# Performance work log

Measured on AMD Instinct MI355X. Metric: run time of the kernel, lower is better.

Reference implementation:

```python
import jax, jax.numpy as jnp
import numpy as np

NEG_INF = -1e9

def setup_inputs() -> dict:
    key = jax.random.key(0)
    ks = jax.random.split(key, 6)
    B, M, RNN, H, D = 64, 1024, 1024, 512, 2048
    return {
        "h": jax.random.normal(ks[0], (B, RNN), dtype=jnp.float32),
        "att_feats": jax.random.normal(ks[1], (B, M, D), dtype=jnp.float32),
        "att_mask": jax.random.randint(ks[2], (B, M), 0, 2, dtype=jnp.int32),
        "p_att_feats": jax.random.normal(ks[3], (B, M, H), dtype=jnp.float32),
        "W_ah": jax.random.normal(ks[4], (H, RNN), dtype=jnp.float32) * (1.0 / np.sqrt(RNN)),
        "w_alpha": jax.random.normal(ks[5], (H,), dtype=jnp.float32) * (1.0 / np.sqrt(H)),
    }

def reference(h, att_feats, att_mask, p_att_feats, W_ah, w_alpha):
    # Wah(h): [B, H]
    wah = h @ W_ah.T
    # additive attention energies: tanh(Wah(h)[:, None, :] + p_att_feats) -> [B, M, H]
    e = jnp.tanh(wah[:, None, :] + p_att_feats)
    # project to scalar per region: [B, M]
    logits = jnp.einsum("bmh,h->bm", e, w_alpha)
    logits = jnp.where(att_mask == 0, NEG_INF, logits)
    alpha = jax.nn.softmax(logits, axis=-1)
    # weighted sum of region features: [B, D]
    att = jnp.einsum("bm,bmd->bd", alpha, att_feats)
    return att
```

## Files before the change

### kernel.cpp

```cpp
#include <hip/hip_runtime.h>
#include <math.h>

#define B   64
#define M   1024
#define RNN 1024
#define H   512
#define D   2048

#define NCHUNK 16
#define CROWS  (M / NCHUNK)
#define RPW    (CROWS / 4)

__device__ __forceinline__ float fast_tanh(float x) {
    float ax = fabsf(x);
    float t  = __expf(-2.0f * ax);
    float r  = (1.0f - t) * __builtin_amdgcn_rcpf(1.0f + t);
    return copysignf(r, x);
}

__global__ __launch_bounds__(256) void k_wah(const float* __restrict__ h,
                                             const float* __restrict__ W,
                                             float* __restrict__ wah) {
    const int tid = threadIdx.x, lane = tid & 63, w = tid >> 6;
    const int bt = blockIdx.y * 16;
    const int j0 = blockIdx.x * 8 + w * 2;

    __shared__ float s_h[16 * RNN];
    const float4* h4  = (const float4*)(h + (size_t)bt * RNN);
    float4*       sh4 = (float4*)s_h;
#pragma unroll
    for (int k = 0; k < 16; ++k)
        sh4[tid + k * 256] = h4[tid + k * 256];

    const float4* Wa = (const float4*)(W + (size_t)j0 * RNN);
    const float4* Wb = (const float4*)(W + (size_t)(j0 + 1) * RNN);
    float4 wa[4], wb[4];
#pragma unroll
    for (int k = 0; k < 4; ++k) { wa[k] = Wa[lane + 64 * k]; wb[k] = Wb[lane + 64 * k]; }
    __syncthreads();

    for (int b = 0; b < 16; ++b) {
        float d0 = 0.0f, d1 = 0.0f;
#pragma unroll
        for (int k = 0; k < 4; ++k) {
            float4 hv = sh4[b * 256 + lane + 64 * k];
            d0 += hv.x * wa[k].x + hv.y * wa[k].y + hv.z * wa[k].z + hv.w * wa[k].w;
            d1 += hv.x * wb[k].x + hv.y * wb[k].y + hv.z * wb[k].z + hv.w * wb[k].w;
        }
#pragma unroll
        for (int off = 32; off > 0; off >>= 1) {
            d0 += __shfl_xor(d0, off);
            d1 += __shfl_xor(d1, off);
        }
        if (lane == 0)
            *(float2*)(wah + (size_t)(bt + b) * H + j0) = make_float2(d0, d1);
    }
}

__global__ __launch_bounds__(256) void k_fused(const float* __restrict__ wah,
                                               const float* __restrict__ p_att,
                                               const int* __restrict__ mask,
                                               const float* __restrict__ w_alpha,
                                               const float* __restrict__ feats,
                                               float* __restrict__ partial,
                                               float* __restrict__ zpart) {
    const int b   = blockIdx.x;
    const int c   = blockIdx.y;
    const int tid = threadIdx.x;
    const int lane = tid & 63;
    const int w    = tid >> 6;

    __shared__ float          s_w[CROWS];
    __shared__ float          s_zred[4];
    __shared__ unsigned short s_idx[CROWS + 4];
    __shared__ float          s_val[CROWS + 4];
    __shared__ int            s_cntreal;

    const float4* wh4 = (const float4*)(wah + (size_t)b * H);
    const float4* wa4 = (const float4*)w_alpha;
    float4 wh0 = wh4[lane], wh1 = wh4[lane + 64];
    float4 wa0 = wa4[lane], wa1 = wa4[lane + 64];

    const int     m0   = c * CROWS;
    const int*    mrow = mask + (size_t)b * M + m0;
    const float4* pb4  = (const float4*)(p_att + ((size_t)b * M + m0) * H);

    float zsum = 0.0f;
    for (int r = w * RPW; r < w * RPW + RPW; ++r) {
        float e = 0.0f;
        if (mrow[r] != 0) {
            float4 p0 = pb4[(size_t)r * (H / 4) + lane];
            float4 p1 = pb4[(size_t)r * (H / 4) + 64 + lane];
            float s = fast_tanh(p0.x + wh0.x) * wa0.x
                    + fast_tanh(p0.y + wh0.y) * wa0.y
                    + fast_tanh(p0.z + wh0.z) * wa0.z
                    + fast_tanh(p0.w + wh0.w) * wa0.w
                    + fast_tanh(p1.x + wh1.x) * wa1.x
                    + fast_tanh(p1.y + wh1.y) * wa1.y
                    + fast_tanh(p1.z + wh1.z) * wa1.z
                    + fast_tanh(p1.w + wh1.w) * wa1.w;
#pragma unroll
            for (int off = 32; off > 0; off >>= 1)
                s += __shfl_xor(s, off);
            e = __expf(s);
        }
        if (lane == 0) s_w[r] = e;
        zsum += e;
    }
    if (lane == 0) s_zred[w] = zsum;
    __syncthreads();
    if (tid == 0)
        zpart[(size_t)c * B + b] = (s_zred[0] + s_zred[1]) + (s_zred[2] + s_zred[3]);

    if (tid < CROWS) {
        float a = s_w[tid];
        bool pred = (a != 0.0f);
        unsigned long long bal = __ballot(pred);
        int pos = __popcll(bal & ((1ull << lane) - 1ull));
        if (pred) { s_idx[pos] = (unsigned short)tid; s_val[pos] = a; }
        if (lane == 0) s_cntreal = __popcll(bal);
    }
    __syncthreads();
    const int cnt = s_cntreal;
    const int n   = (cnt + 3) & ~3;
    if (tid >= cnt && tid < n) {
        s_idx[tid] = (cnt > 0) ? s_idx[cnt - 1] : (unsigned short)0;
        s_val[tid] = 0.0f;
    }
    __syncthreads();

    const float4* fb4 = (const float4*)(feats + ((size_t)b * M + m0) * D)
                        + (size_t)w * 128 + lane;
    float4 acc0 = {0.f, 0.f, 0.f, 0.f}, acc1 = {0.f, 0.f, 0.f, 0.f};
    for (int i = 0; i < n; i += 4) {
        int   r0 = s_idx[i],     r1 = s_idx[i + 1];
        int   r2 = s_idx[i + 2], r3 = s_idx[i + 3];
        float v0 = s_val[i],     v1 = s_val[i + 1];
        float v2 = s_val[i + 2], v3 = s_val[i + 3];
        const float4* q0 = fb4 + (size_t)r0 * (D / 4);
        const float4* q1 = fb4 + (size_t)r1 * (D / 4);
        const float4* q2 = fb4 + (size_t)r2 * (D / 4);
        const float4* q3 = fb4 + (size_t)r3 * (D / 4);
        float4 f00 = q0[0], f01 = q0[64];
        float4 f10 = q1[0], f11 = q1[64];
        float4 f20 = q2[0], f21 = q2[64];
        float4 f30 = q3[0], f31 = q3[64];
        acc0.x += v0 * f00.x; acc0.y += v0 * f00.y; acc0.z += v0 * f00.z; acc0.w += v0 * f00.w;
        acc1.x += v0 * f01.x; acc1.y += v0 * f01.y; acc1.z += v0 * f01.z; acc1.w += v0 * f01.w;
        acc0.x += v1 * f10.x; acc0.y += v1 * f10.y; acc0.z += v1 * f10.z; acc0.w += v1 * f10.w;
        acc1.x += v1 * f11.x; acc1.y += v1 * f11.y; acc1.z += v1 * f11.z; acc1.w += v1 * f11.w;
        acc0.x += v2 * f20.x; acc0.y += v2 * f20.y; acc0.z += v2 * f20.z; acc0.w += v2 * f20.w;
        acc1.x += v2 * f21.x; acc1.y += v2 * f21.y; acc1.z += v2 * f21.z; acc1.w += v2 * f21.w;
        acc0.x += v3 * f30.x; acc0.y += v3 * f30.y; acc0.z += v3 * f30.z; acc0.w += v3 * f30.w;
        acc1.x += v3 * f31.x; acc1.y += v3 * f31.y; acc1.z += v3 * f31.z; acc1.w += v3 * f31.w;
    }
    float4* ob = (float4*)(partial + ((size_t)c * B + b) * D) + (size_t)w * 128 + lane;
    ob[0]  = acc0;
    ob[64] = acc1;
}

__global__ __launch_bounds__(256) void k_reduce(const float* __restrict__ partial,
                                                const float* __restrict__ zpart,
                                                float* __restrict__ out) {
    int i4 = blockIdx.x * 256 + threadIdx.x;
    int b  = i4 >> 9;
    float Z = 0.0f;
#pragma unroll
    for (int c = 0; c < NCHUNK; ++c)
        Z += zpart[c * B + b];
    const float4* p4 = (const float4*)partial;
    float4 s = p4[i4];
#pragma unroll
    for (int c = 1; c < NCHUNK; ++c) {
        float4 v = p4[(size_t)c * (B * D / 4) + i4];
        s.x += v.x; s.y += v.y; s.z += v.z; s.w += v.w;
    }
    float inv = 1.0f / Z;
    float4 r = {s.x * inv, s.y * inv, s.z * inv, s.w * inv};
    ((float4*)out)[i4] = r;
}

extern "C" void kernel_launch(void* const* d_in, const int* in_sizes, int n_in,
                              void* d_out, int out_size, void* d_ws, size_t ws_size,
                              hipStream_t stream) {
    const float* h       = (const float*)d_in[0];
    const float* feats   = (const float*)d_in[1];
    const int*   mask    = (const int*)d_in[2];
    const float* p_att   = (const float*)d_in[3];
    const float* W_ah    = (const float*)d_in[4];
    const float* w_alpha = (const float*)d_in[5];
    float* out = (float*)d_out;

    float* ws      = (float*)d_ws;
    float* wah     = ws;
    float* zpart   = wah + B * H;
    float* partial = zpart + NCHUNK * B;

    k_wah   <<<dim3(H / 8, B / 16), 256, 0, stream>>>(h, W_ah, wah);
    k_fused <<<dim3(B, NCHUNK), 256, 0, stream>>>(wah, p_att, mask, w_alpha, feats,
                                                  partial, zpart);
    k_reduce<<<dim3(B * D / 1024), 256, 0, stream>>>(partial, zpart, out);
}
```

Before: 78.63 us.

## Fuse feature gather into the score loop with per-wave full-row accumulation

The fused kernel now issues the att_feats row loads alongside the p_att loads and accumulates e*feats inside the same per-row loop. Each wave owns whole rows and keeps 32 accumulator floats per lane across all of D, and the four waves are combined through a 32KB shared-memory reduction. This removes the two-phase scheme with its score buffer, ballot compaction and extra barriers, and overlaps feature loads with the tanh work. In exchange, register pressure and shared memory rise (launch bounds now ask for 4 blocks), and each wave walks its rows serially.

```diff
diff --git a/kernel.cpp b/kernel.cpp
--- a/kernel.cpp
+++ b/kernel.cpp
@@ -57,24 +57,21 @@
     }
 }
 
-__global__ __launch_bounds__(256) void k_fused(const float* __restrict__ wah,
-                                               const float* __restrict__ p_att,
-                                               const int* __restrict__ mask,
-                                               const float* __restrict__ w_alpha,
-                                               const float* __restrict__ feats,
-                                               float* __restrict__ partial,
-                                               float* __restrict__ zpart) {
+__global__ __launch_bounds__(256, 4) void k_fused(const float* __restrict__ wah,
+                                                  const float* __restrict__ p_att,
+                                                  const int* __restrict__ mask,
+                                                  const float* __restrict__ w_alpha,
+                                                  const float* __restrict__ feats,
+                                                  float* __restrict__ partial,
+                                                  float* __restrict__ zpart) {
     const int b   = blockIdx.x;
     const int c   = blockIdx.y;
     const int tid = threadIdx.x;
     const int lane = tid & 63;
     const int w    = tid >> 6;
 
-    __shared__ float          s_w[CROWS];
-    __shared__ float          s_zred[4];
-    __shared__ unsigned short s_idx[CROWS + 4];
-    __shared__ float          s_val[CROWS + 4];
-    __shared__ int            s_cntreal;
+    __shared__ float s_acc[4][D];
+    __shared__ float s_z[4];
 
     const float4* wh4 = (const float4*)(wah + (size_t)b * H);
     const float4* wa4 = (const float4*)w_alpha;
@@ -84,79 +81,60 @@
     const int     m0   = c * CROWS;
     const int*    mrow = mask + (size_t)b * M + m0;
     const float4* pb4  = (const float4*)(p_att + ((size_t)b * M + m0) * H);
+    const float4* fb4  = (const float4*)(feats + ((size_t)b * M + m0) * D);
 
+    float4 acc[8];
+#pragma unroll
+    for (int j = 0; j < 8; ++j) acc[j] = make_float4(0.f, 0.f, 0.f, 0.f);
     float zsum = 0.0f;
+
     for (int r = w * RPW; r < w * RPW + RPW; ++r) {
-        float e = 0.0f;
-        if (mrow[r] != 0) {
-            float4 p0 = pb4[(size_t)r * (H / 4) + lane];
-            float4 p1 = pb4[(size_t)r * (H / 4) + 64 + lane];
-            float s = fast_tanh(p0.x + wh0.x) * wa0.x
-                    + fast_tanh(p0.y + wh0.y) * wa0.y
-                    + fast_tanh(p0.z + wh0.z) * wa0.z
-                    + fast_tanh(p0.w + wh0.w) * wa0.w
-                    + fast_tanh(p1.x + wh1.x) * wa1.x
-                    + fast_tanh(p1.y + wh1.y) * wa1.y
-                    + fast_tanh(p1.z + wh1.z) * wa1.z
-                    + fast_tanh(p1.w + wh1.w) * wa1.w;
+        if (mrow[r] == 0) continue;
+        const float4* pr = pb4 + (size_t)r * (H / 4);
+        const float4* fr = fb4 + (size_t)r * (D / 4) + lane;
+        float4 p0 = pr[lane], p1 = pr[lane + 64];
+        float4 f0 = fr[0],   f1 = fr[64],  f2 = fr[128], f3 = fr[192];
+        float4 f4 = fr[256], f5 = fr[320], f6 = fr[384], f7 = fr[448];
+
+        float s = fast_tanh(p0.x + wh0.x) * wa0.x
+                + fast_tanh(p0.y + wh0.y) * wa0.y
+                + fast_tanh(p0.z + wh0.z) * wa0.z
+                + fast_tanh(p0.w + wh0.w) * wa0.w
+                + fast_tanh(p1.x + wh1.x) * wa1.x
+                + fast_tanh(p1.y + wh1.y) * wa1.y
+                + fast_tanh(p1.z + wh1.z) * wa1.z
+                + fast_tanh(p1.w + wh1.w) * wa1.w;
 #pragma unroll
-            for (int off = 32; off > 0; off >>= 1)
-                s += __shfl_xor(s, off);
-            e = __expf(s);
-        }
-        if (lane == 0) s_w[r] = e;
+        for (int off = 32; off > 0; off >>= 1)
+            s += __shfl_xor(s, off);
+        float e = __expf(s);
         zsum += e;
+
+        acc[0].x += e * f0.x; acc[0].y += e * f0.y; acc[0].z += e * f0.z; acc[0].w += e * f0.w;
+        acc[1].x += e * f1.x; acc[1].y += e * f1.y; acc[1].z += e * f1.z; acc[1].w += e * f1.w;
+        acc[2].x += e * f2.x; acc[2].y += e * f2.y; acc[2].z += e * f2.z; acc[2].w += e * f2.w;
+        acc[3].x += e * f3.x; acc[3].y += e * f3.y; acc[3].z += e * f3.z; acc[3].w += e * f3.w;
+        acc[4].x += e * f4.x; acc[4].y += e * f4.y; acc[4].z += e * f4.z; acc[4].w += e * f4.w;
+        acc[5].x += e * f5.x; acc[5].y += e * f5.y; acc[5].z += e * f5.z; acc[5].w += e * f5.w;
+        acc[6].x += e * f6.x; acc[6].y += e * f6.y; acc[6].z += e * f6.z; acc[6].w += e * f6.w;
+        acc[7].x += e * f7.x; acc[7].y += e * f7.y; acc[7].z += e * f7.z; acc[7].w += e * f7.w;
     }
-    if (lane == 0) s_zred[w] = zsum;
-    __syncthreads();
-    if (tid == 0)
-        zpart[(size_t)c * B + b] = (s_zred[0] + s_zred[1]) + (s_zred[2] + s_zred[3]);
 
-    if (tid < CROWS) {
-        float a = s_w[tid];
-        bool pred = (a != 0.0f);
-        unsigned long long bal = __ballot(pred);
-        int pos = __popcll(bal & ((1ull << lane) - 1ull));
-        if (pred) { s_idx[pos] = (unsigned short)tid; s_val[pos] = a; }
-        if (lane == 0) s_cntreal = __popcll(bal);
-    }
-    __syncthreads();
-    const int cnt = s_cntreal;
-    const int n   = (cnt + 3) & ~3;
-    if (tid >= cnt && tid < n) {
-        s_idx[tid] = (cnt > 0) ? s_idx[cnt - 1] : (unsigned short)0;
-        s_val[tid] = 0.0f;
-    }
+#pragma unroll
+    for (int j = 0; j < 8; ++j)
+        *(float4*)&s_acc[w][j * 256 + lane * 4] = acc[j];
+    if (lane == 0) s_z[w] = zsum;
     __syncthreads();
 
-    const float4* fb4 = (const float4*)(feats + ((size_t)b * M + m0) * D)
-                        + (size_t)w * 128 + lane;
-    float4 acc0 = {0.f, 0.f, 0.f, 0.f}, acc1 = {0.f, 0.f, 0.f, 0.f};
-    for (int i = 0; i < n; i += 4) {
-        int   r0 = s_idx[i],     r1 = s_idx[i + 1];
-        int   r2 = s_idx[i + 2], r3 = s_idx[i + 3];
-        float v0 = s_val[i],     v1 = s_val[i + 1];
-        float v2 = s_val[i + 2], v3 = s_val[i + 3];
-        const float4* q0 = fb4 + (size_t)r0 * (D / 4);
-        const float4* q1 = fb4 + (size_t)r1 * (D / 4);
-        const float4* q2 = fb4 + (size_t)r2 * (D / 4);
-        const float4* q3 = fb4 + (size_t)r3 * (D / 4);
-        float4 f00 = q0[0], f01 = q0[64];
-        float4 f10 = q1[0], f11 = q1[64];
-        float4 f20 = q2[0], f21 = q2[64];
-        float4 f30 = q3[0], f31 = q3[64];
-        acc0.x += v0 * f00.x; acc0.y += v0 * f00.y; acc0.z += v0 * f00.z; acc0.w += v0 * f00.w;
-        acc1.x += v0 * f01.x; acc1.y += v0 * f01.y; acc1.z += v0 * f01.z; acc1.w += v0 * f01.w;
-        acc0.x += v1 * f10.x; acc0.y += v1 * f10.y; acc0.z += v1 * f10.z; acc0.w += v1 * f10.w;
-        acc1.x += v1 * f11.x; acc1.y += v1 * f11.y; acc1.z += v1 * f11.z; acc1.w += v1 * f11.w;
-        acc0.x += v2 * f20.x; acc0.y += v2 * f20.y; acc0.z += v2 * f20.z; acc0.w += v2 * f20.w;
-        acc1.x += v2 * f21.x; acc1.y += v2 * f21.y; acc1.z += v2 * f21.z; acc1.w += v2 * f21.w;
-        acc0.x += v3 * f30.x; acc0.y += v3 * f30.y; acc0.z += v3 * f30.z; acc0.w += v3 * f30.w;
-        acc1.x += v3 * f31.x; acc1.y += v3 * f31.y; acc1.z += v3 * f31.z; acc1.w += v3 * f31.w;
+    if (tid == 0)
+        zpart[(size_t)c * B + b] = (s_z[0] + s_z[1]) + (s_z[2] + s_z[3]);
+
+    float* pout = partial + ((size_t)c * B + b) * D;
+#pragma unroll
+    for (int k = 0; k < 8; ++k) {
+        int d = k * 256 + tid;
+        pout[d] = (s_acc[0][d] + s_acc[1][d]) + (s_acc[2][d] + s_acc[3][d]);
     }
-    float4* ob = (float4*)(partial + ((size_t)c * B + b) * D) + (size_t)w * 128 + lane;
-    ob[0]  = acc0;
-    ob[64] = acc1;
 }
 
 __global__ __launch_bounds__(256) void k_reduce(const float* __restrict__ partial,
```

Result: faster. 76.69 us (-2.5%).
